# Kernel optimization log

Measured on AMD Instinct MI355X. Metric: run time of the kernel, lower is better.

Reference implementation:

```python
import jax, jax.numpy as jnp
import numpy as np

INPUT_DIM = 128
HIDDEN_DIM = 128
WINDOW_SIZE = 256
BLOCK_SIZE = 256
BATCH = 8
SEQ = 8192


def setup_inputs() -> dict:
    key = jax.random.key(0)
    ks = jax.random.split(key, 7)
    s = 1.0 / np.sqrt(INPUT_DIM)
    return {
        "x": jax.random.normal(ks[0], (BATCH, SEQ, INPUT_DIM), dtype=jnp.float32),
        "Wq": jax.random.normal(ks[1], (HIDDEN_DIM, INPUT_DIM), dtype=jnp.float32) * s,
        "bq": jax.random.normal(ks[2], (HIDDEN_DIM,), dtype=jnp.float32) * s,
        "Wk": jax.random.normal(ks[3], (HIDDEN_DIM, INPUT_DIM), dtype=jnp.float32) * s,
        "bk": jax.random.normal(ks[4], (HIDDEN_DIM,), dtype=jnp.float32) * s,
        "Wv": jax.random.normal(ks[5], (HIDDEN_DIM, INPUT_DIM), dtype=jnp.float32) * s,
        "bv": jax.random.normal(ks[6], (HIDDEN_DIM,), dtype=jnp.float32) * s,
    }


def reference(x, Wq, bq, Wk, bk, Wv, bv):
    B, S, D = x.shape
    bs, w = BLOCK_SIZE, WINDOW_SIZE
    nb = S // bs
    halo = w - 1
    W = bs + 2 * halo  # per-block K/V window width

    q = x @ Wq.T + bq  # [B,S,H]
    k = x @ Wk.T + bk
    v = x @ Wv.T + bv

    # Zero-pad K/V by halo on both sides. Since there is NO softmax, padded
    # zero keys give zero scores and padded zero values contribute zero —
    # this exactly reproduces the torch code's clamped window slicing.
    k_pad = jnp.pad(k, ((0, 0), (halo, halo), (0, 0)))
    v_pad = jnp.pad(v, ((0, 0), (halo, halo), (0, 0)))

    # Gather overlapping windows: [B, nb, W, H]
    starts = jnp.arange(nb) * bs  # window start in padded coords
    idx = starts[:, None] + jnp.arange(W)[None, :]  # [nb, W]
    k_win = k_pad[:, idx, :]
    v_win = v_pad[:, idx, :]

    q_blk = q.reshape(B, nb, bs, -1)  # [B, nb, bs, H]

    scale = 1.0 / jnp.sqrt(jnp.float32(D))
    attn = jnp.einsum('bnqh,bnkh->bnqk', q_blk, k_win) * scale  # no softmax
    out = jnp.einsum('bnqk,bnkh->bnqh', attn, v_win)
    return out.reshape(B, S, -1)
```

## Files before the change

kernel.cpp:

```cpp
#include <hip/hip_runtime.h>
#include <stdint.h>


#define B_ 8
#define S_ 8192
#define LDW 136
#define LDT 264

using bf16x8 = __attribute__((ext_vector_type(8))) short;
using s16x4  = __attribute__((ext_vector_type(4))) short;
using f32x16 = __attribute__((ext_vector_type(16))) float;

__device__ __forceinline__ short f2bf(float f) {
  union { float f; uint32_t u; } v; v.f = f;
  uint32_t r = v.u + 0x7fffu + ((v.u >> 16) & 1u);
  return (short)(r >> 16);
}
__device__ __forceinline__ float bf2f(short s) {
  union { uint32_t u; float f; } v; v.u = ((uint32_t)(uint16_t)s) << 16;
  return v.f;
}

__global__ __launch_bounds__(512) void kv_kernel(
    const float* __restrict__ x,
    const float* __restrict__ Wk, const float* __restrict__ bk,
    const float* __restrict__ Wv, const float* __restrict__ bv,
    float* __restrict__ Cpart, short* __restrict__ kedge,
    short* __restrict__ vedge)
{
  __shared__ short bufK[128 * LDT];
  __shared__ short bufV[128 * LDT];

  const int tid  = threadIdx.x;
  const int lane = tid & 63;
  const int wv   = tid >> 6;
  const int c    = lane & 31;
  const int hl   = lane >> 5;
  const int r0   = blockIdx.x * 256;
  const int b    = r0 >> 13;
  const int n    = (r0 & (S_ - 1)) >> 8;

  bf16x8 afrag[8];
  {
    const float* xrow = x + (size_t)(r0 + wv * 32 + c) * 128 + hl * 8;
    #pragma unroll
    for (int kst = 0; kst < 8; ++kst) {
      const float4* p = (const float4*)(xrow + kst * 16);
      float4 f0 = p[0], f1 = p[1];
      bf16x8 a;
      a[0] = f2bf(f0.x); a[1] = f2bf(f0.y); a[2] = f2bf(f0.z); a[3] = f2bf(f0.w);
      a[4] = f2bf(f1.x); a[5] = f2bf(f1.y); a[6] = f2bf(f1.z); a[7] = f2bf(f1.w);
      afrag[kst] = a;
    }
  }

  auto stageW = [&](const float* W, short* wl) {
    #pragma unroll
    for (int it = 0; it < 8; ++it) {
      int l  = it * 512 + tid;
      int nn = l >> 5;
      int k4 = (l & 31) << 2;
      const float4 f = *(const float4*)(W + nn * 128 + k4);
      s16x4 o;
      o[0] = f2bf(f.x); o[1] = f2bf(f.y); o[2] = f2bf(f.z); o[3] = f2bf(f.w);
      *(s16x4*)(wl + nn * LDW + k4) = o;
    }
  };

  auto gemm = [&](const float* bias, f32x16* acc, const short* wl) {
    #pragma unroll
    for (int nt = 0; nt < 4; ++nt) {
      float bvv = bias[nt * 32 + c];
      #pragma unroll
      for (int i = 0; i < 16; ++i) acc[nt][i] = bvv;
    }
    #pragma unroll
    for (int kst = 0; kst < 8; ++kst) {
      #pragma unroll
      for (int nt = 0; nt < 4; ++nt) {
        bf16x8 bb = *(const bf16x8*)(wl + (nt * 32 + c) * LDW + kst * 16 + hl * 8);
        acc[nt] = __builtin_amdgcn_mfma_f32_32x32x16_bf16(afrag[kst], bb, acc[nt], 0, 0, 0);
      }
    }
  };

  auto writeTransposedLDS = [&](f32x16* acc, short* wl) {
    #pragma unroll
    for (int nt = 0; nt < 4; ++nt) {
      int d = nt * 32 + c;
      #pragma unroll
      for (int g = 0; g < 4; ++g) {
        #pragma unroll
        for (int p = 0; p < 2; ++p) {
          int reg = g * 4 + p * 2;
          int sl  = wv * 32 + g * 8 + hl * 4 + p * 2;
          uint32_t pk = (uint32_t)(uint16_t)f2bf(acc[nt][reg]) |
                        ((uint32_t)(uint16_t)f2bf(acc[nt][reg + 1]) << 16);
          *(uint32_t*)(wl + d * LDT + sl) = pk;
        }
      }
    }
  };

  stageW(Wk, bufK);
  __syncthreads();
  {
    f32x16 acc[4];
    gemm(bk, acc, bufK);
    __syncthreads();
    writeTransposedLDS(acc, bufK);
    stageW(Wv, bufV);
  }
  __syncthreads();

  {
    f32x16 acc[4];
    gemm(bv, acc, bufV);
    __syncthreads();
    writeTransposedLDS(acc, bufV);
  }
  __syncthreads();

  {
    const int ht = wv >> 1;
    const int dh = wv & 1;
    f32x16 cacc[2];
    #pragma unroll
    for (int t = 0; t < 2; ++t)
      #pragma unroll
      for (int i = 0; i < 16; ++i) cacc[t][i] = 0.f;

    #pragma unroll
    for (int kst = 0; kst < 16; ++kst) {
      bf16x8 a  = *(const bf16x8*)(bufV + (ht * 32 + c) * LDT + kst * 16 + hl * 8);
      bf16x8 b0 = *(const bf16x8*)(bufK + (dh * 64 + c) * LDT + kst * 16 + hl * 8);
      bf16x8 b1 = *(const bf16x8*)(bufK + (dh * 64 + 32 + c) * LDT + kst * 16 + hl * 8);
      cacc[0] = __builtin_amdgcn_mfma_f32_32x32x16_bf16(a, b0, cacc[0], 0, 0, 0);
      cacc[1] = __builtin_amdgcn_mfma_f32_32x32x16_bf16(a, b1, cacc[1], 0, 0, 0);
    }

    {
      size_t eo = ((size_t)(b * 32 + n)) * 256;
      if (tid < 128)      kedge[eo + tid]               = bufK[tid * LDT + 0];
      else if (tid < 256) kedge[eo + 128 + (tid - 128)] = bufK[(tid - 128) * LDT + 255];
      else if (tid < 384) vedge[eo + (tid - 256)]       = bufV[(tid - 256) * LDT + 0];
      else                vedge[eo + 128 + (tid - 384)] = bufV[(tid - 384) * LDT + 255];
    }

    float* Cp = Cpart + ((size_t)(b * 32 + n)) * 16384;
    #pragma unroll
    for (int t = 0; t < 2; ++t) {
      #pragma unroll
      for (int reg = 0; reg < 16; ++reg) {
        int row = (reg & 3) + 8 * (reg >> 2) + 4 * hl;
        Cp[(ht * 32 + row) * 128 + dh * 64 + t * 32 + c] = cacc[t][reg];
      }
    }
  }
}

__global__ __launch_bounds__(512) void qattn_kernel(
    const float* __restrict__ x,
    const float* __restrict__ Wq, const float* __restrict__ bq,
    const float* __restrict__ Cpart,
    const short* __restrict__ kedge, const short* __restrict__ vedge,
    float* __restrict__ out)
{
  __shared__ __align__(16) char smem[71680];
  short* q_l  = (short*)smem;
  short* m_l  = (short*)smem;
  float* opat = (float*)(smem + 34816);

  const int tid  = threadIdx.x;
  const int lane = tid & 63;
  const int wv   = tid >> 6;
  const int c    = lane & 31;
  const int hl   = lane >> 5;
  const int r0   = blockIdx.x * 256;
  const int b    = r0 >> 13;
  const int n    = (r0 & (S_ - 1)) >> 8;

  bf16x8 afrag[8];
  {
    const float* xrow = x + (size_t)(r0 + wv * 32 + c) * 128 + hl * 8;
    #pragma unroll
    for (int kst = 0; kst < 8; ++kst) {
      const float4* p = (const float4*)(xrow + kst * 16);
      float4 f0 = p[0], f1 = p[1];
      bf16x8 a;
      a[0] = f2bf(f0.x); a[1] = f2bf(f0.y); a[2] = f2bf(f0.z); a[3] = f2bf(f0.w);
      a[4] = f2bf(f1.x); a[5] = f2bf(f1.y); a[6] = f2bf(f1.z); a[7] = f2bf(f1.w);
      afrag[kst] = a;
    }
  }

  #pragma unroll
  for (int it = 0; it < 8; ++it) {
    int l  = it * 512 + tid;
    int nn = l >> 5;
    int k4 = (l & 31) << 2;
    const float4 f = *(const float4*)(Wq + nn * 128 + k4);
    s16x4 o;
    o[0] = f2bf(f.x); o[1] = f2bf(f.y); o[2] = f2bf(f.z); o[3] = f2bf(f.w);
    *(s16x4*)(q_l + nn * LDW + k4) = o;
  }
  __syncthreads();

  f32x16 qacc[4];
  #pragma unroll
  for (int nt = 0; nt < 4; ++nt) {
    float bvv = bq[nt * 32 + c];
    #pragma unroll
    for (int i = 0; i < 16; ++i) qacc[nt][i] = bvv;
  }
  #pragma unroll
  for (int kst = 0; kst < 8; ++kst) {
    #pragma unroll
    for (int nt = 0; nt < 4; ++nt) {
      bf16x8 bb = *(const bf16x8*)(q_l + (nt * 32 + c) * LDW + kst * 16 + hl * 8);
      qacc[nt] = __builtin_amdgcn_mfma_f32_32x32x16_bf16(afrag[kst], bb, qacc[nt], 0, 0, 0);
    }
  }
  __syncthreads();

  #pragma unroll
  for (int nt = 0; nt < 4; ++nt) {
    #pragma unroll
    for (int reg = 0; reg < 16; ++reg) {
      int row = (reg & 3) + 8 * (reg >> 2) + 4 * hl;
      q_l[(wv * 32 + row) * LDW + nt * 32 + c] = f2bf(qacc[nt][reg]);
    }
  }
  __syncthreads();

  bf16x8 qf[8];
  #pragma unroll
  for (int kst = 0; kst < 8; ++kst)
    qf[kst] = *(const bf16x8*)(q_l + (wv * 32 + c) * LDW + kst * 16 + hl * 8);

  float m[32];
  #pragma unroll
  for (int i = 0; i < 32; ++i) m[i] = 0.f;

  const float* Cb0 = Cpart + (size_t)b * 32 * 16384;
  #pragma unroll
  for (int e = 0; e < 3; ++e) {
    int nn = n - 1 + e;
    if (nn < 0 || nn > 31) continue;
    const float4* Cp = (const float4*)(Cb0 + (size_t)nn * 16384);
    #pragma unroll
    for (int i4 = 0; i4 < 8; ++i4) {
      float4 f = Cp[i4 * 512 + tid];
      m[i4 * 4 + 0] += f.x; m[i4 * 4 + 1] += f.y;
      m[i4 * 4 + 2] += f.z; m[i4 * 4 + 3] += f.w;
    }
  }

  const int d0 = (tid & 31) << 2;
  if (n > 0) {
    const short* ke = kedge + ((size_t)(b * 32 + n - 1)) * 256;
    const short* ve = vedge + ((size_t)(b * 32 + n - 1)) * 256;
    float k0 = bf2f(ke[d0]),     k1 = bf2f(ke[d0 + 1]);
    float k2 = bf2f(ke[d0 + 2]), k3 = bf2f(ke[d0 + 3]);
    #pragma unroll
    for (int i4 = 0; i4 < 8; ++i4) {
      float vs = bf2f(ve[i4 * 16 + (tid >> 5)]);
      m[i4 * 4 + 0] -= vs * k0; m[i4 * 4 + 1] -= vs * k1;
      m[i4 * 4 + 2] -= vs * k2; m[i4 * 4 + 3] -= vs * k3;
    }
  }
  if (n < 31) {
    const short* ke = kedge + ((size_t)(b * 32 + n + 1)) * 256 + 128;
    const short* ve = vedge + ((size_t)(b * 32 + n + 1)) * 256 + 128;
    float k0 = bf2f(ke[d0]),     k1 = bf2f(ke[d0 + 1]);
    float k2 = bf2f(ke[d0 + 2]), k3 = bf2f(ke[d0 + 3]);
    #pragma unroll
    for (int i4 = 0; i4 < 8; ++i4) {
      float vs = bf2f(ve[i4 * 16 + (tid >> 5)]);
      m[i4 * 4 + 0] -= vs * k0; m[i4 * 4 + 1] -= vs * k1;
      m[i4 * 4 + 2] -= vs * k2; m[i4 * 4 + 3] -= vs * k3;
    }
  }
  __syncthreads();

  const float scale = 0.08838834764831845f;
  #pragma unroll
  for (int i4 = 0; i4 < 8; ++i4) {
    int h = i4 * 16 + (tid >> 5);
    s16x4 o;
    o[0] = f2bf(m[i4 * 4 + 0] * scale); o[1] = f2bf(m[i4 * 4 + 1] * scale);
    o[2] = f2bf(m[i4 * 4 + 2] * scale); o[3] = f2bf(m[i4 * 4 + 3] * scale);
    *(s16x4*)(m_l + h * LDW + d0) = o;
  }
  __syncthreads();

  f32x16 oacc[4];
  #pragma unroll
  for (int nt = 0; nt < 4; ++nt)
    #pragma unroll
    for (int i = 0; i < 16; ++i) oacc[nt][i] = 0.f;

  #pragma unroll
  for (int kst = 0; kst < 8; ++kst) {
    #pragma unroll
    for (int nt = 0; nt < 4; ++nt) {
      bf16x8 bb = *(const bf16x8*)(m_l + (nt * 32 + c) * LDW + kst * 16 + hl * 8);
      oacc[nt] = __builtin_amdgcn_mfma_f32_32x32x16_bf16(qf[kst], bb, oacc[nt], 0, 0, 0);
    }
  }

  float* patch = opat + wv * (32 * 36);
  float* outb  = out + ((size_t)b * S_ + n * 256 + wv * 32) * 128;
  #pragma unroll
  for (int nt = 0; nt < 4; ++nt) {
    #pragma unroll
    for (int reg = 0; reg < 16; ++reg) {
      int row = (reg & 3) + 8 * (reg >> 2) + 4 * hl;
      patch[row * 36 + c] = oacc[nt][reg];
    }
    #pragma unroll
    for (int p = 0; p < 4; ++p) {
      int row = p * 8 + (lane >> 3);
      float4 vv = *(const float4*)(patch + row * 36 + (lane & 7) * 4);
      *(float4*)(outb + (size_t)row * 128 + nt * 32 + (lane & 7) * 4) = vv;
    }
  }
}

extern "C" void kernel_launch(void* const* d_in, const int* in_sizes, int n_in,
                              void* d_out, int out_size, void* d_ws, size_t ws_size,
                              hipStream_t stream) {
  const float* x  = (const float*)d_in[0];
  const float* Wq = (const float*)d_in[1];
  const float* bq = (const float*)d_in[2];
  const float* Wk = (const float*)d_in[3];
  const float* bk = (const float*)d_in[4];
  const float* Wv = (const float*)d_in[5];
  const float* bv = (const float*)d_in[6];
  float* out = (float*)d_out;

  float* Cpart = (float*)d_ws;
  short* kedge = (short*)(Cpart + (size_t)8 * 32 * 16384);
  short* vedge = kedge + (size_t)8 * 32 * 256;

  kv_kernel<<<256, 512, 0, stream>>>(x, Wk, bk, Wv, bv, Cpart, kedge, vedge);
  qattn_kernel<<<256, 512, 0, stream>>>(x, Wq, bq, Cpart, kedge, vedge, out);
}
```

Baseline: 120.4 us.

## Move Q projection into KV kernel and pass bf16 Q through workspace

The Q projection now runs in the first kernel, which already holds x fragments in registers, so x no longer has to be reloaded and converted in the second kernel. Q is written to global memory as bf16 and read back by a slimmed attention kernel, which now only builds the M matrix and does the final GEMM. The first kernel does more work and uses larger LDS (two reused regions of about 137KB total), while the second gets lighter with smaller LDS and one fewer barrier. This trades one extra global round trip of bf16 Q for avoiding a second full-precision read of x and a second weight staging.

```diff
diff --git a/kernel.cpp b/kernel.cpp
--- a/kernel.cpp
+++ b/kernel.cpp
@@ -23,13 +23,15 @@
 
 __global__ __launch_bounds__(512) void kv_kernel(
     const float* __restrict__ x,
+    const float* __restrict__ Wq, const float* __restrict__ bq,
     const float* __restrict__ Wk, const float* __restrict__ bk,
     const float* __restrict__ Wv, const float* __restrict__ bv,
-    float* __restrict__ Cpart, short* __restrict__ kedge,
-    short* __restrict__ vedge)
+    short* __restrict__ qb, float* __restrict__ Cpart,
+    short* __restrict__ kedge, short* __restrict__ vedge)
 {
-  __shared__ short bufK[128 * LDT];
-  __shared__ short bufV[128 * LDT];
+  __shared__ __align__(16) char smem[137216];
+  short* rgA = (short*)smem;
+  short* rgB = (short*)(smem + 69632);
 
   const int tid  = threadIdx.x;
   const int lane = tid & 63;
@@ -102,23 +104,44 @@
     }
   };
 
-  stageW(Wk, bufK);
-  __syncthreads();
-  {
-    f32x16 acc[4];
-    gemm(bk, acc, bufK);
-    __syncthreads();
-    writeTransposedLDS(acc, bufK);
-    stageW(Wv, bufV);
-  }
-  __syncthreads();
-
-  {
-    f32x16 acc[4];
-    gemm(bv, acc, bufV);
-    __syncthreads();
-    writeTransposedLDS(acc, bufV);
-  }
+  stageW(Wq, rgA);
+  __syncthreads();
+  f32x16 qacc[4];
+  gemm(bq, qacc, rgA);
+  __syncthreads();
+
+  #pragma unroll
+  for (int nt = 0; nt < 4; ++nt) {
+    #pragma unroll
+    for (int reg = 0; reg < 16; ++reg) {
+      int row = (reg & 3) + 8 * (reg >> 2) + 4 * hl;
+      rgA[(wv * 32 + row) * LDW + nt * 32 + c] = f2bf(qacc[nt][reg]);
+    }
+  }
+  stageW(Wk, rgB);
+  __syncthreads();
+
+  #pragma unroll
+  for (int it = 0; it < 8; ++it) {
+    int l  = it * 512 + tid;
+    int s  = l >> 4;
+    int d8 = (l & 15) << 3;
+    bf16x8 vvv = *(const bf16x8*)(rgA + s * LDW + d8);
+    *(bf16x8*)(qb + (size_t)(r0 + s) * 128 + d8) = vvv;
+  }
+  f32x16 kacc[4];
+  gemm(bk, kacc, rgB);
+  __syncthreads();
+
+  writeTransposedLDS(kacc, rgA);
+  stageW(Wv, rgB);
+  __syncthreads();
+
+  f32x16 vacc[4];
+  gemm(bv, vacc, rgB);
+  __syncthreads();
+
+  writeTransposedLDS(vacc, rgB);
   __syncthreads();
 
   {
@@ -132,19 +155,19 @@
 
     #pragma unroll
     for (int kst = 0; kst < 16; ++kst) {
-      bf16x8 a  = *(const bf16x8*)(bufV + (ht * 32 + c) * LDT + kst * 16 + hl * 8);
-      bf16x8 b0 = *(const bf16x8*)(bufK + (dh * 64 + c) * LDT + kst * 16 + hl * 8);
-      bf16x8 b1 = *(const bf16x8*)(bufK + (dh * 64 + 32 + c) * LDT + kst * 16 + hl * 8);
+      bf16x8 a  = *(const bf16x8*)(rgB + (ht * 32 + c) * LDT + kst * 16 + hl * 8);
+      bf16x8 b0 = *(const bf16x8*)(rgA + (dh * 64 + c) * LDT + kst * 16 + hl * 8);
+      bf16x8 b1 = *(const bf16x8*)(rgA + (dh * 64 + 32 + c) * LDT + kst * 16 + hl * 8);
       cacc[0] = __builtin_amdgcn_mfma_f32_32x32x16_bf16(a, b0, cacc[0], 0, 0, 0);
       cacc[1] = __builtin_amdgcn_mfma_f32_32x32x16_bf16(a, b1, cacc[1], 0, 0, 0);
     }
 
     {
       size_t eo = ((size_t)(b * 32 + n)) * 256;
-      if (tid < 128)      kedge[eo + tid]               = bufK[tid * LDT + 0];
-      else if (tid < 256) kedge[eo + 128 + (tid - 128)] = bufK[(tid - 128) * LDT + 255];
-      else if (tid < 384) vedge[eo + (tid - 256)]       = bufV[(tid - 256) * LDT + 0];
-      else                vedge[eo + 128 + (tid - 384)] = bufV[(tid - 384) * LDT + 255];
+      if (tid < 128)      kedge[eo + tid]               = rgA[tid * LDT + 0];
+      else if (tid < 256) kedge[eo + 128 + (tid - 128)] = rgA[(tid - 128) * LDT + 255];
+      else if (tid < 384) vedge[eo + (tid - 256)]       = rgB[(tid - 256) * LDT + 0];
+      else                vedge[eo + 128 + (tid - 384)] = rgB[(tid - 384) * LDT + 255];
     }
 
     float* Cp = Cpart + ((size_t)(b * 32 + n)) * 16384;
@@ -159,17 +182,13 @@
   }
 }
 
-__global__ __launch_bounds__(512) void qattn_kernel(
-    const float* __restrict__ x,
-    const float* __restrict__ Wq, const float* __restrict__ bq,
-    const float* __restrict__ Cpart,
+__global__ __launch_bounds__(512) void attn_kernel(
+    const short* __restrict__ qb, const float* __restrict__ Cpart,
     const short* __restrict__ kedge, const short* __restrict__ vedge,
     float* __restrict__ out)
 {
-  __shared__ __align__(16) char smem[71680];
-  short* q_l  = (short*)smem;
-  short* m_l  = (short*)smem;
-  float* opat = (float*)(smem + 34816);
+  __shared__ __align__(16) short m_l[128 * LDW];
+  __shared__ __align__(16) float opat[8 * 32 * 36];
 
   const int tid  = threadIdx.x;
   const int lane = tid & 63;
@@ -180,64 +199,6 @@
   const int b    = r0 >> 13;
   const int n    = (r0 & (S_ - 1)) >> 8;
 
-  bf16x8 afrag[8];
-  {
-    const float* xrow = x + (size_t)(r0 + wv * 32 + c) * 128 + hl * 8;
-    #pragma unroll
-    for (int kst = 0; kst < 8; ++kst) {
-      const float4* p = (const float4*)(xrow + kst * 16);
-      float4 f0 = p[0], f1 = p[1];
-      bf16x8 a;
-      a[0] = f2bf(f0.x); a[1] = f2bf(f0.y); a[2] = f2bf(f0.z); a[3] = f2bf(f0.w);
-      a[4] = f2bf(f1.x); a[5] = f2bf(f1.y); a[6] = f2bf(f1.z); a[7] = f2bf(f1.w);
-      afrag[kst] = a;
-    }
-  }
-
-  #pragma unroll
-  for (int it = 0; it < 8; ++it) {
-    int l  = it * 512 + tid;
-    int nn = l >> 5;
-    int k4 = (l & 31) << 2;
-    const float4 f = *(const float4*)(Wq + nn * 128 + k4);
-    s16x4 o;
-    o[0] = f2bf(f.x); o[1] = f2bf(f.y); o[2] = f2bf(f.z); o[3] = f2bf(f.w);
-    *(s16x4*)(q_l + nn * LDW + k4) = o;
-  }
-  __syncthreads();
-
-  f32x16 qacc[4];
-  #pragma unroll
-  for (int nt = 0; nt < 4; ++nt) {
-    float bvv = bq[nt * 32 + c];
-    #pragma unroll
-    for (int i = 0; i < 16; ++i) qacc[nt][i] = bvv;
-  }
-  #pragma unroll
-  for (int kst = 0; kst < 8; ++kst) {
-    #pragma unroll
-    for (int nt = 0; nt < 4; ++nt) {
-      bf16x8 bb = *(const bf16x8*)(q_l + (nt * 32 + c) * LDW + kst * 16 + hl * 8);
-      qacc[nt] = __builtin_amdgcn_mfma_f32_32x32x16_bf16(afrag[kst], bb, qacc[nt], 0, 0, 0);
-    }
-  }
-  __syncthreads();
-
-  #pragma unroll
-  for (int nt = 0; nt < 4; ++nt) {
-    #pragma unroll
-    for (int reg = 0; reg < 16; ++reg) {
-      int row = (reg & 3) + 8 * (reg >> 2) + 4 * hl;
-      q_l[(wv * 32 + row) * LDW + nt * 32 + c] = f2bf(qacc[nt][reg]);
-    }
-  }
-  __syncthreads();
-
-  bf16x8 qf[8];
-  #pragma unroll
-  for (int kst = 0; kst < 8; ++kst)
-    qf[kst] = *(const bf16x8*)(q_l + (wv * 32 + c) * LDW + kst * 16 + hl * 8);
-
   float m[32];
   #pragma unroll
   for (int i = 0; i < 32; ++i) m[i] = 0.f;
@@ -281,7 +242,6 @@
       m[i4 * 4 + 2] -= vs * k2; m[i4 * 4 + 3] -= vs * k3;
     }
   }
-  __syncthreads();
 
   const float scale = 0.08838834764831845f;
   #pragma unroll
@@ -291,6 +251,13 @@
     o[0] = f2bf(m[i4 * 4 + 0] * scale); o[1] = f2bf(m[i4 * 4 + 1] * scale);
     o[2] = f2bf(m[i4 * 4 + 2] * scale); o[3] = f2bf(m[i4 * 4 + 3] * scale);
     *(s16x4*)(m_l + h * LDW + d0) = o;
+  }
+
+  bf16x8 qf[8];
+  {
+    const short* q0p = qb + (size_t)(r0 + wv * 32 + c) * 128 + hl * 8;
+    #pragma unroll
+    for (int kst = 0; kst < 8; ++kst) qf[kst] = *(const bf16x8*)(q0p + kst * 16);
   }
   __syncthreads();
 
@@ -342,7 +309,9 @@
   float* Cpart = (float*)d_ws;
   short* kedge = (short*)(Cpart + (size_t)8 * 32 * 16384);
   short* vedge = kedge + (size_t)8 * 32 * 256;
-
-  kv_kernel<<<256, 512, 0, stream>>>(x, Wk, bk, Wv, bv, Cpart, kedge, vedge);
-  qattn_kernel<<<256, 512, 0, stream>>>(x, Wq, bq, Cpart, kedge, vedge, out);
-}
+  short* qb    = vedge + (size_t)8 * 32 * 256;
+
+  kv_kernel<<<256, 512, 0, stream>>>(x, Wq, bq, Wk, bk, Wv, bv,
+                                     qb, Cpart, kedge, vedge);
+  attn_kernel<<<256, 512, 0, stream>>>(qb, Cpart, kedge, vedge, out);
+}
```

Measured after the change: 118.5 us. Within noise of the previous version (-1.5%).

## Fold Wq into per-block KV matrix and remap block order to XCDs

Applied to the files above, without the earlier changes.

The attention kernel no longer forms Q explicitly. It multiplies the 128x128 per-block M matrix by Wq to get N = M·Wq, then computes x·N plus a bias term bq·M reduced with wave shuffles. This replaces the per-row Q projection GEMM and Q re-layout with a single small 128x128 GEMM per block. The KV kernel now stages Wk and Wv together and runs both GEMMs back-to-back with fewer barriers, at the cost of more LDS. Both kernels remap blockIdx so consecutive blocks land on the same XCD, which may improve L2 locality for the neighbouring-block Cpart reads.

```diff
diff --git a/kernel.cpp b/kernel.cpp
--- a/kernel.cpp
+++ b/kernel.cpp
@@ -28,15 +28,17 @@
     float* __restrict__ Cpart, short* __restrict__ kedge,
     short* __restrict__ vedge)
 {
-  __shared__ short bufK[128 * LDT];
-  __shared__ short bufV[128 * LDT];
+  __shared__ __align__(16) char smem[135168];
+  short* areaA = (short*)smem;
+  short* areaB = (short*)(smem + 67584);
 
   const int tid  = threadIdx.x;
   const int lane = tid & 63;
   const int wv   = tid >> 6;
   const int c    = lane & 31;
   const int hl   = lane >> 5;
-  const int r0   = blockIdx.x * 256;
+  const int wg   = ((int)blockIdx.x & 7) * 32 + ((int)blockIdx.x >> 3);
+  const int r0   = wg * 256;
   const int b    = r0 >> 13;
   const int n    = (r0 & (S_ - 1)) >> 8;
 
@@ -102,23 +104,17 @@
     }
   };
 
-  stageW(Wk, bufK);
-  __syncthreads();
-  {
-    f32x16 acc[4];
-    gemm(bk, acc, bufK);
-    __syncthreads();
-    writeTransposedLDS(acc, bufK);
-    stageW(Wv, bufV);
-  }
-  __syncthreads();
-
-  {
-    f32x16 acc[4];
-    gemm(bv, acc, bufV);
-    __syncthreads();
-    writeTransposedLDS(acc, bufV);
-  }
+  stageW(Wk, areaA);
+  stageW(Wv, areaB);
+  __syncthreads();
+
+  f32x16 kacc[4], vacc[4];
+  gemm(bk, kacc, areaA);
+  gemm(bv, vacc, areaB);
+  __syncthreads();
+
+  writeTransposedLDS(kacc, areaA);
+  writeTransposedLDS(vacc, areaB);
   __syncthreads();
 
   {
@@ -132,19 +128,19 @@
 
     #pragma unroll
     for (int kst = 0; kst < 16; ++kst) {
-      bf16x8 a  = *(const bf16x8*)(bufV + (ht * 32 + c) * LDT + kst * 16 + hl * 8);
-      bf16x8 b0 = *(const bf16x8*)(bufK + (dh * 64 + c) * LDT + kst * 16 + hl * 8);
-      bf16x8 b1 = *(const bf16x8*)(bufK + (dh * 64 + 32 + c) * LDT + kst * 16 + hl * 8);
+      bf16x8 a  = *(const bf16x8*)(areaB + (ht * 32 + c) * LDT + kst * 16 + hl * 8);
+      bf16x8 b0 = *(const bf16x8*)(areaA + (dh * 64 + c) * LDT + kst * 16 + hl * 8);
+      bf16x8 b1 = *(const bf16x8*)(areaA + (dh * 64 + 32 + c) * LDT + kst * 16 + hl * 8);
       cacc[0] = __builtin_amdgcn_mfma_f32_32x32x16_bf16(a, b0, cacc[0], 0, 0, 0);
       cacc[1] = __builtin_amdgcn_mfma_f32_32x32x16_bf16(a, b1, cacc[1], 0, 0, 0);
     }
 
     {
       size_t eo = ((size_t)(b * 32 + n)) * 256;
-      if (tid < 128)      kedge[eo + tid]               = bufK[tid * LDT + 0];
-      else if (tid < 256) kedge[eo + 128 + (tid - 128)] = bufK[(tid - 128) * LDT + 255];
-      else if (tid < 384) vedge[eo + (tid - 256)]       = bufV[(tid - 256) * LDT + 0];
-      else                vedge[eo + 128 + (tid - 384)] = bufV[(tid - 384) * LDT + 255];
+      if (tid < 128)      kedge[eo + tid]               = areaA[tid * LDT + 0];
+      else if (tid < 256) kedge[eo + 128 + (tid - 128)] = areaA[(tid - 128) * LDT + 255];
+      else if (tid < 384) vedge[eo + (tid - 256)]       = areaB[(tid - 256) * LDT + 0];
+      else                vedge[eo + 128 + (tid - 384)] = areaB[(tid - 384) * LDT + 255];
     }
 
     float* Cp = Cpart + ((size_t)(b * 32 + n)) * 16384;
@@ -159,24 +155,27 @@
   }
 }
 
-__global__ __launch_bounds__(512) void qattn_kernel(
+__global__ __launch_bounds__(512) void attn_kernel(
     const float* __restrict__ x,
     const float* __restrict__ Wq, const float* __restrict__ bq,
     const float* __restrict__ Cpart,
     const short* __restrict__ kedge, const short* __restrict__ vedge,
     float* __restrict__ out)
 {
-  __shared__ __align__(16) char smem[71680];
-  short* q_l  = (short*)smem;
-  short* m_l  = (short*)smem;
-  float* opat = (float*)(smem + 34816);
+  __shared__ __align__(16) char smem[104960];
+  short* wqT   = (short*)smem;
+  short* m_l   = (short*)(smem + 34816);
+  short* n_l   = (short*)(smem + 69632);
+  float* bqM_l = (float*)(smem + 104448);
+  float* opat  = (float*)smem;
 
   const int tid  = threadIdx.x;
   const int lane = tid & 63;
   const int wv   = tid >> 6;
   const int c    = lane & 31;
   const int hl   = lane >> 5;
-  const int r0   = blockIdx.x * 256;
+  const int wg   = ((int)blockIdx.x & 7) * 32 + ((int)blockIdx.x >> 3);
+  const int r0   = wg * 256;
   const int b    = r0 >> 13;
   const int n    = (r0 & (S_ - 1)) >> 8;
 
@@ -197,46 +196,14 @@
   #pragma unroll
   for (int it = 0; it < 8; ++it) {
     int l  = it * 512 + tid;
-    int nn = l >> 5;
-    int k4 = (l & 31) << 2;
-    const float4 f = *(const float4*)(Wq + nn * 128 + k4);
-    s16x4 o;
-    o[0] = f2bf(f.x); o[1] = f2bf(f.y); o[2] = f2bf(f.z); o[3] = f2bf(f.w);
-    *(s16x4*)(q_l + nn * LDW + k4) = o;
-  }
-  __syncthreads();
-
-  f32x16 qacc[4];
-  #pragma unroll
-  for (int nt = 0; nt < 4; ++nt) {
-    float bvv = bq[nt * 32 + c];
-    #pragma unroll
-    for (int i = 0; i < 16; ++i) qacc[nt][i] = bvv;
-  }
-  #pragma unroll
-  for (int kst = 0; kst < 8; ++kst) {
-    #pragma unroll
-    for (int nt = 0; nt < 4; ++nt) {
-      bf16x8 bb = *(const bf16x8*)(q_l + (nt * 32 + c) * LDW + kst * 16 + hl * 8);
-      qacc[nt] = __builtin_amdgcn_mfma_f32_32x32x16_bf16(afrag[kst], bb, qacc[nt], 0, 0, 0);
-    }
-  }
-  __syncthreads();
-
-  #pragma unroll
-  for (int nt = 0; nt < 4; ++nt) {
-    #pragma unroll
-    for (int reg = 0; reg < 16; ++reg) {
-      int row = (reg & 3) + 8 * (reg >> 2) + 4 * hl;
-      q_l[(wv * 32 + row) * LDW + nt * 32 + c] = f2bf(qacc[nt][reg]);
-    }
-  }
-  __syncthreads();
-
-  bf16x8 qf[8];
-  #pragma unroll
-  for (int kst = 0; kst < 8; ++kst)
-    qf[kst] = *(const bf16x8*)(q_l + (wv * 32 + c) * LDW + kst * 16 + hl * 8);
+    int f  = l >> 5;
+    int d4 = (l & 31) << 2;
+    const float4 w = *(const float4*)(Wq + f * 128 + d4);
+    wqT[(d4 + 0) * LDW + f] = f2bf(w.x);
+    wqT[(d4 + 1) * LDW + f] = f2bf(w.y);
+    wqT[(d4 + 2) * LDW + f] = f2bf(w.z);
+    wqT[(d4 + 3) * LDW + f] = f2bf(w.w);
+  }
 
   float m[32];
   #pragma unroll
@@ -281,16 +248,57 @@
       m[i4 * 4 + 2] -= vs * k2; m[i4 * 4 + 3] -= vs * k3;
     }
   }
-  __syncthreads();
 
   const float scale = 0.08838834764831845f;
+  float4 bqv = *(const float4*)(bq + d0);
+  float bp[8];
   #pragma unroll
   for (int i4 = 0; i4 < 8; ++i4) {
     int h = i4 * 16 + (tid >> 5);
+    float m0 = m[i4 * 4 + 0] * scale, m1 = m[i4 * 4 + 1] * scale;
+    float m2 = m[i4 * 4 + 2] * scale, m3 = m[i4 * 4 + 3] * scale;
     s16x4 o;
-    o[0] = f2bf(m[i4 * 4 + 0] * scale); o[1] = f2bf(m[i4 * 4 + 1] * scale);
-    o[2] = f2bf(m[i4 * 4 + 2] * scale); o[3] = f2bf(m[i4 * 4 + 3] * scale);
+    o[0] = f2bf(m0); o[1] = f2bf(m1); o[2] = f2bf(m2); o[3] = f2bf(m3);
     *(s16x4*)(m_l + h * LDW + d0) = o;
+    bp[i4] = m0 * bqv.x + m1 * bqv.y + m2 * bqv.z + m3 * bqv.w;
+  }
+  #pragma unroll
+  for (int mask = 1; mask <= 16; mask <<= 1) {
+    #pragma unroll
+    for (int i4 = 0; i4 < 8; ++i4) bp[i4] += __shfl_xor(bp[i4], mask);
+  }
+  if ((tid & 31) == 0) {
+    #pragma unroll
+    for (int i4 = 0; i4 < 8; ++i4) bqM_l[i4 * 16 + (tid >> 5)] = bp[i4];
+  }
+  __syncthreads();
+
+  {
+    const int ht2 = wv >> 1;
+    const int dc  = (wv & 1) * 64;
+    f32x16 nacc[2];
+    #pragma unroll
+    for (int t = 0; t < 2; ++t)
+      #pragma unroll
+      for (int i = 0; i < 16; ++i) nacc[t][i] = 0.f;
+
+    #pragma unroll
+    for (int kst = 0; kst < 8; ++kst) {
+      bf16x8 a = *(const bf16x8*)(m_l + (ht2 * 32 + c) * LDW + kst * 16 + hl * 8);
+      #pragma unroll
+      for (int t = 0; t < 2; ++t) {
+        bf16x8 bb = *(const bf16x8*)(wqT + (dc + t * 32 + c) * LDW + kst * 16 + hl * 8);
+        nacc[t] = __builtin_amdgcn_mfma_f32_32x32x16_bf16(a, bb, nacc[t], 0, 0, 0);
+      }
+    }
+    #pragma unroll
+    for (int t = 0; t < 2; ++t) {
+      #pragma unroll
+      for (int reg = 0; reg < 16; ++reg) {
+        int row = (reg & 3) + 8 * (reg >> 2) + 4 * hl;
+        n_l[(ht2 * 32 + row) * LDW + dc + t * 32 + c] = f2bf(nacc[t][reg]);
+      }
+    }
   }
   __syncthreads();
 
@@ -304,19 +312,20 @@
   for (int kst = 0; kst < 8; ++kst) {
     #pragma unroll
     for (int nt = 0; nt < 4; ++nt) {
-      bf16x8 bb = *(const bf16x8*)(m_l + (nt * 32 + c) * LDW + kst * 16 + hl * 8);
-      oacc[nt] = __builtin_amdgcn_mfma_f32_32x32x16_bf16(qf[kst], bb, oacc[nt], 0, 0, 0);
+      bf16x8 bb = *(const bf16x8*)(n_l + (nt * 32 + c) * LDW + kst * 16 + hl * 8);
+      oacc[nt] = __builtin_amdgcn_mfma_f32_32x32x16_bf16(afrag[kst], bb, oacc[nt], 0, 0, 0);
     }
   }
 
   float* patch = opat + wv * (32 * 36);
-  float* outb  = out + ((size_t)b * S_ + n * 256 + wv * 32) * 128;
+  float* outb  = out + ((size_t)r0 + wv * 32) * 128;
   #pragma unroll
   for (int nt = 0; nt < 4; ++nt) {
+    float bias = bqM_l[nt * 32 + c];
     #pragma unroll
     for (int reg = 0; reg < 16; ++reg) {
       int row = (reg & 3) + 8 * (reg >> 2) + 4 * hl;
-      patch[row * 36 + c] = oacc[nt][reg];
+      patch[row * 36 + c] = oacc[nt][reg] + bias;
     }
     #pragma unroll
     for (int p = 0; p < 4; ++p) {
@@ -344,5 +353,5 @@
   short* vedge = kedge + (size_t)8 * 32 * 256;
 
   kv_kernel<<<256, 512, 0, stream>>>(x, Wk, bk, Wv, bv, Cpart, kedge, vedge);
-  qattn_kernel<<<256, 512, 0, stream>>>(x, Wq, bq, Cpart, kedge, vedge, out);
-}
+  attn_kernel<<<256, 512, 0, stream>>>(x, Wq, bq, Cpart, kedge, vedge, out);
+}
```

After: 117.1 us, median of 2. 2.7% less time.
